# Performance work log

Measured on AMD Instinct MI355X. Metric: run time of the kernel, lower is better.

Reference implementation:

```python
import jax, jax.numpy as jnp
import numpy as np

B, SEQ, V = 8, 2048, 4096
D, H, DH, NL, FF = 1024, 16, 64, 8, 4096
MAXLEN = 4096
ATTN_EPS = 1e-6


def setup_inputs() -> dict:
    key = jax.random.key(0)
    ks = iter(jax.random.split(key, 40))
    w = lambda *s: jax.random.normal(next(ks), s, jnp.float32) * 0.02
    z = lambda *s: jnp.zeros(s, jnp.float32)
    o = lambda *s: jnp.ones(s, jnp.float32)
    return {
        'inputs': jax.random.uniform(next(ks), (B, SEQ, V), jnp.float32),
        'We': w(V, D), 'be': z(D),          # embedding Linear (stored [in,out])
        'pos': w(MAXLEN, D),                # positional embedding table
        'Wq': w(NL, D, D), 'bq': z(NL, D),
        'Wk': w(NL, D, D), 'bk': z(NL, D),
        'Wv': w(NL, D, D), 'bv': z(NL, D),
        'Wo': w(NL, D, D), 'bo': z(NL, D),
        'ln1g': o(NL, D), 'ln1b': z(NL, D),
        'W1': w(NL, D, FF), 'b1': z(NL, FF),
        'W2': w(NL, FF, D), 'b2': z(NL, D),
        'ln2g': o(NL, D), 'ln2b': z(NL, D),
        'gN': o(D), 'bN': z(D),
        'Wout': w(D, V), 'bout': z(V),
    }


def _rotate_half(u):
    u1, u2 = jnp.split(u, 2, axis=-1)
    return jnp.concatenate([-u2, u1], axis=-1)


def _ln(u, g, b, eps=1e-5):
    m = u.mean(-1, keepdims=True)
    var = ((u - m) ** 2).mean(-1, keepdims=True)
    return (u - m) * jax.lax.rsqrt(var + eps) * g + b


def _forward(inputs, We, be, pos, Wq, bq, Wk, bk, Wv, bv, Wo, bo,
             ln1g, ln1b, W1, b1, W2, b2, ln2g, ln2b, gN, bN, Wout, bout):
    N, S, Vv = inputs.shape
    T = S + 1
    # CLS one-hot prepended (last vocab slot reserved for CLS)
    cls = jnp.zeros((N, 1, Vv), inputs.dtype).at[:, :, Vv - 1].set(1.0)
    x = jnp.concatenate([cls, inputs], axis=1)       # [N,T,V]
    x = x @ We + be + pos[:T][None]                  # [N,T,D]

    # rotary tables for head_dim DH
    inv_freq = 1.0 / (10000.0 ** (jnp.arange(0, DH, 2, dtype=jnp.float32) / DH))
    freqs = jnp.arange(T, dtype=jnp.float32)[:, None] * inv_freq[None, :]
    emb = jnp.concatenate([freqs, freqs], axis=-1)   # [T,DH]
    cos = jnp.cos(emb)[None, :, None, :]
    sin = jnp.sin(emb)[None, :, None, :]

    def layer(x, p):
        wq, bq_, wk, bk_, wv, bv_, wo, bo_, g1, b1_, w1, bf1, w2, bf2, g2, b2_ = p
        q = (x @ wq + bq_).reshape(N, T, H, DH)
        k = (x @ wk + bk_).reshape(N, T, H, DH)
        v = (x @ wv + bv_).reshape(N, T, H, DH)
        q = q * cos + _rotate_half(q) * sin
        k = k * cos + _rotate_half(k) * sin
        # linear (kernelized) attention: phi(x) = elu(x) + 1, non-causal
        Qf = jax.nn.elu(q) + 1.0
        Kf = jax.nn.elu(k) + 1.0
        KV = jnp.einsum('nshd,nshm->nhdm', Kf, v)            # [N,H,DH,DH]
        Z = 1.0 / (jnp.einsum('nlhd,nhd->nlh', Qf, Kf.sum(1)) + ATTN_EPS)
        attn = jnp.einsum('nlhd,nhdm,nlh->nlhm', Qf, KV, Z).reshape(N, T, D)
        x = _ln(x + attn @ wo + bo_, g1, b1_)
        ff = jax.nn.gelu(x @ w1 + bf1, approximate=False) @ w2 + bf2
        x = _ln(x + ff, g2, b2_)
        return x, None

    params = (Wq, bq, Wk, bk, Wv, bv, Wo, bo, ln1g, ln1b, W1, b1, W2, b2, ln2g, ln2b)
    x, _ = jax.lax.scan(layer, x, params)
    x = _ln(x, gN, bN)
    return x[:, 0] @ Wout + bout                     # [N,V]


def reference(inputs, We, be, pos, Wq, bq, Wk, bk, Wv, bv, Wo, bo,
              ln1g, ln1b, W1, b1, W2, b2, ln2g, ln2b, gN, bN, Wout, bout):
    return _forward(inputs, We, be, pos, Wq, bq, Wk, bk, Wv, bv, Wo, bo,
                    ln1g, ln1b, W1, b1, W2, b2, ln2g, ln2b, gN, bN, Wout, bout)
```

## Files before the change

kernel.cpp:

```cpp
#include <hip/hip_runtime.h>
#include <math.h>

#define NB 8
#define SEQ 2048
#define V 4096
#define D 1024
#define H 16
#define DH 64
#define NL 8
#define FF 4096
#define TVAL 2049
#define MVAL (NB*TVAL)
#define MPAD 16512
#define TS 2112

typedef unsigned short u16;
typedef __attribute__((ext_vector_type(8))) __bf16 bfrag;
typedef __attribute__((ext_vector_type(4))) float f32x4;
typedef __attribute__((ext_vector_type(8))) unsigned short us8;
typedef __attribute__((ext_vector_type(4))) float fvec4;

__device__ __forceinline__ float b2f(u16 u) {
  union { unsigned int i; float f; } x; x.i = ((unsigned int)u) << 16; return x.f;
}
__device__ __forceinline__ u16 f2b(float f) {
  union { float f; unsigned int i; } x; x.f = f;
  unsigned int r = x.i + 0x7FFFu + ((x.i >> 16) & 1u);
  return (u16)(r >> 16);
}
__device__ __forceinline__ float phi_fn(float x) { return x > 0.f ? x + 1.f : __expf(x); }

__device__ __forceinline__ void async16(const u16* g, u16* l) {
  auto gp = (const __attribute__((address_space(1))) unsigned int*)(unsigned long long)g;
  auto lp = (__attribute__((address_space(3))) unsigned int*)(unsigned int)(unsigned long long)l;
  __builtin_amdgcn_global_load_lds(gp, lp, 16, 0, 0);
}

__device__ __forceinline__ f32x4 mfma16(bfrag a, bfrag b, f32x4 c) {
  return __builtin_amdgcn_mfma_f32_16x16x32_bf16(a, b, c, 0, 0, 0);
}


__global__ __launch_bounds__(256) void conv_kernel(const float* __restrict__ src,
                                                   u16* __restrict__ dst, long n) {
  long i = ((long)blockIdx.x * 256 + threadIdx.x) * 4;
  if (i < n) {
    fvec4 v = *(const fvec4*)(src + i);
    u16 o[4];
    #pragma unroll
    for (int j = 0; j < 4; ++j) o[j] = f2b(v[j]);
    *(uint2*)(dst + i) = *(const uint2*)o;
  }
}

__global__ __launch_bounds__(256) void transposeW(const float* __restrict__ src,
                                                  u16* __restrict__ dst, int K, int N) {
  const int z = blockIdx.z;
  src += (size_t)z * K * N;
  dst += (size_t)z * K * N;
  const int k0 = blockIdx.x * 64, n0 = blockIdx.y * 64;
  __shared__ __align__(16) u16 t[64][65];
  const int c = threadIdx.x & 63, r4 = threadIdx.x >> 6;
  #pragma unroll 4
  for (int i = 0; i < 16; ++i) {
    int k = i * 4 + r4;
    t[c][k] = f2b(src[(size_t)(k0 + k) * N + n0 + c]);
  }
  __syncthreads();
  #pragma unroll 4
  for (int i = 0; i < 16; ++i) {
    int nr = i * 4 + r4;
    dst[(size_t)(n0 + nr) * K + k0 + c] = t[nr][c];
  }
}

__global__ __launch_bounds__(256) void rope_table(float* __restrict__ ct, float* __restrict__ snt) {
  int idx = blockIdx.x * 256 + threadIdx.x;
  if (idx < TVAL * 32) {
    int s = idx >> 5, p = idx & 31;
    float ang = (float)s * powf(10000.f, -(float)p / 32.f);
    ct[idx] = cosf(ang);
    snt[idx] = sinf(ang);
  }
}

__global__ __launch_bounds__(256) void cls_kernel(const float* __restrict__ We,
                                                  const float* __restrict__ be,
                                                  const float* __restrict__ pos,
                                                  u16* __restrict__ xb, float* __restrict__ xf) {
  int n = blockIdx.x;
  for (int c = threadIdx.x; c < D; c += 256) {
    float v = We[(size_t)(V - 1) * D + c] + be[c] + pos[c];
    size_t idx = (size_t)(n * TVAL) * D + c;
    xb[idx] = f2b(v);
    xf[idx] = v;
  }
}

template<int EPI>
__global__ __launch_bounds__(256) void gemm_bt(
    const u16* __restrict__ A, const u16* __restrict__ Bt,
    const float* __restrict__ bias, const float* __restrict__ resf,
    const float* __restrict__ pos, u16* __restrict__ Cb, float* __restrict__ Cf,
    int N, int K) {
  __shared__ __align__(16) u16 sA[4096];
  __shared__ __align__(16) u16 sB[4096];
  const int tid = threadIdx.x, wave = tid >> 6, lane = tid & 63;
  const int fr = lane & 15, fc8 = (lane >> 4) << 3;
  const int rA = blockIdx.y * 128, rB = blockIdx.x * 128;
  const u16* gA0 = A + (size_t)(rA + wave * 16 + fr) * K + fc8;
  const u16* gA1 = A + (size_t)(rA + 64 + wave * 16 + fr) * K + fc8;
  const u16* gB0 = Bt + (size_t)(rB + wave * 16 + fr) * K + fc8;
  const u16* gB1 = Bt + (size_t)(rB + 64 + wave * 16 + fr) * K + fc8;
  u16* lA0 = sA + wave * 512;
  u16* lA1 = sA + (4 + wave) * 512;
  u16* lB0 = sB + wave * 512;
  u16* lB1 = sB + (4 + wave) * 512;
  const int wm = wave & 1, wn = wave >> 1;
  f32x4 acc[4][4];
  #pragma unroll
  for (int mt = 0; mt < 4; ++mt)
    #pragma unroll
    for (int nt = 0; nt < 4; ++nt)
      #pragma unroll
      for (int r = 0; r < 4; ++r) acc[mt][nt][r] = 0.f;

  for (int kk = 0; kk < K; kk += 32) {
    __syncthreads();
    async16(gA0 + kk, lA0);
    async16(gA1 + kk, lA1);
    async16(gB0 + kk, lB0);
    async16(gB1 + kk, lB1);
    __syncthreads();
    bfrag af[4], bfr[4];
    #pragma unroll
    for (int t = 0; t < 4; ++t) af[t] = *(const bfrag*)(sA + (wm * 4 + t) * 512 + lane * 8);
    #pragma unroll
    for (int t = 0; t < 4; ++t) bfr[t] = *(const bfrag*)(sB + (wn * 4 + t) * 512 + lane * 8);
    #pragma unroll
    for (int mt = 0; mt < 4; ++mt)
      #pragma unroll
      for (int nt = 0; nt < 4; ++nt)
        acc[mt][nt] = mfma16(af[mt], bfr[nt], acc[mt][nt]);
  }

  const int r0 = rA + wm * 64;
  const int c0 = rB + wn * 64;
  #pragma unroll
  for (int mt = 0; mt < 4; ++mt) {
    #pragma unroll
    for (int nt = 0; nt < 4; ++nt) {
      int col = c0 + nt * 16 + fr;
      float bi = bias[col];
      f32x4 v = acc[mt][nt];
      #pragma unroll
      for (int r = 0; r < 4; ++r) {
        int row = r0 + mt * 16 + ((lane >> 4) << 2) + r;
        float val = v[r] + bi;
        if (EPI == 0) {
          int bidx = row >> 11;
          int s = row & 2047;
          size_t orow = (size_t)bidx * TVAL + s + 1;
          float tt = val + pos[(size_t)(s + 1) * D + col];
          Cb[orow * D + col] = f2b(tt);
          Cf[orow * D + col] = tt;
        } else if (EPI == 1) {
          Cb[(size_t)row * N + col] = f2b(val);
        } else if (EPI == 2) {
          Cf[(size_t)row * N + col] = val + resf[(size_t)row * N + col];
        } else {
          float gl = 0.5f * val * (1.f + erff(val * 0.70710678118f));
          Cb[(size_t)row * N + col] = f2b(gl);
        }
      }
    }
  }
}

__global__ __launch_bounds__(256) void rope_kernel(
    u16* qb, const u16* __restrict__ kb, const u16* __restrict__ vb,
    u16* __restrict__ Kt, u16* __restrict__ Vt,
    const float* __restrict__ ct, const float* __restrict__ snt) {
  const int stile = blockIdx.x, h = blockIdx.y, n = blockIdx.z;
  const int tid = threadIdx.x;
  const int sl = tid >> 2;
  const int g8 = (tid & 3) << 3;
  const int s = stile * 64 + sl;
  const bool valid = s < TVAL;
  const size_t row = (size_t)n * TVAL + s;
  float ql[8], qh[8], kl[8], kh[8];
  us8 vlo = {0,0,0,0,0,0,0,0}, vhi = {0,0,0,0,0,0,0,0};
  if (valid) {
    const u16* qp = qb + row * D + (size_t)h * DH;
    const u16* kp = kb + row * D + (size_t)h * DH;
    const u16* vp = vb + row * D + (size_t)h * DH;
    us8 a = *(const us8*)(qp + g8);
    us8 b = *(const us8*)(qp + 32 + g8);
    us8 c = *(const us8*)(kp + g8);
    us8 d = *(const us8*)(kp + 32 + g8);
    vlo = *(const us8*)(vp + g8);
    vhi = *(const us8*)(vp + 32 + g8);
    #pragma unroll
    for (int j = 0; j < 8; ++j) {
      ql[j] = b2f(a[j]); qh[j] = b2f(b[j]);
      kl[j] = b2f(c[j]); kh[j] = b2f(d[j]);
    }
  } else {
    #pragma unroll
    for (int j = 0; j < 8; ++j) { ql[j] = qh[j] = kl[j] = kh[j] = 0.f; }
  }
  const int se = valid ? s : 0;
  us8 qolo, qohi;
  u16 kolo[8], kohi[8];
  #pragma unroll
  for (int j = 0; j < 8; ++j) {
    float c = ct[se * 32 + g8 + j];
    float sn = snt[se * 32 + g8 + j];
    float x1 = ql[j] * c - qh[j] * sn;
    float x2 = qh[j] * c + ql[j] * sn;
    qolo[j] = f2b(phi_fn(x1));
    qohi[j] = f2b(phi_fn(x2));
    float y1 = kl[j] * c - kh[j] * sn;
    float y2 = kh[j] * c + kl[j] * sn;
    kolo[j] = f2b(phi_fn(y1));
    kohi[j] = f2b(phi_fn(y2));
  }
  if (valid) {
    u16* qp = qb + row * D + (size_t)h * DH;
    *(us8*)(qp + g8) = qolo;
    *(us8*)(qp + 32 + g8) = qohi;
  }
  __shared__ __align__(16) u16 tile[64][72];
  #pragma unroll
  for (int j = 0; j < 8; ++j) {
    tile[g8 + j][sl] = valid ? kolo[j] : (u16)0;
    tile[32 + g8 + j][sl] = valid ? kohi[j] : (u16)0;
  }
  __syncthreads();
  {
    const int dr = tid >> 2, ck = (tid & 3) << 4;
    const size_t ob = ((size_t)(n * H + h) * DH + dr) * TS + (size_t)stile * 64 + ck;
    us8 t0 = *(const us8*)&tile[dr][ck];
    us8 t1 = *(const us8*)&tile[dr][ck + 8];
    *(us8*)(Kt + ob) = t0;
    *(us8*)(Kt + ob + 8) = t1;
  }
  __syncthreads();
  #pragma unroll
  for (int j = 0; j < 8; ++j) {
    tile[g8 + j][sl] = valid ? vlo[j] : (u16)0;
    tile[32 + g8 + j][sl] = valid ? vhi[j] : (u16)0;
  }
  __syncthreads();
  {
    const int dr = tid >> 2, ck = (tid & 3) << 4;
    const size_t ob = ((size_t)(n * H + h) * DH + dr) * TS + (size_t)stile * 64 + ck;
    us8 t0 = *(const us8*)&tile[dr][ck];
    us8 t1 = *(const us8*)&tile[dr][ck + 8];
    *(us8*)(Vt + ob) = t0;
    *(us8*)(Vt + ob + 8) = t1;
  }
}

__global__ __launch_bounds__(256) void kv_kernel(
    const u16* __restrict__ Kt, const u16* __restrict__ Vt,
    u16* __restrict__ KVt, float* __restrict__ Ksum) {
  const int nh = blockIdx.x;
  const int tid = threadIdx.x, wave = tid >> 6, lane = tid & 63;
  const size_t base = (size_t)nh * DH * TS;
  const int fr = lane & 15, fc = (lane >> 4) << 3;
  f32x4 acc[4][4];
  #pragma unroll
  for (int a = 0; a < 4; ++a)
    #pragma unroll
    for (int b = 0; b < 4; ++b)
      #pragma unroll
      for (int r = 0; r < 4; ++r) acc[a][b][r] = 0.f;
  for (int c = wave; c < TS / 32; c += 4) {
    const int s0 = c * 32 + fc;
    bfrag av[4], bk[4];
    #pragma unroll
    for (int t = 0; t < 4; ++t) {
      av[t] = *(const bfrag*)(Vt + base + (size_t)(t * 16 + fr) * TS + s0);
      bk[t] = *(const bfrag*)(Kt + base + (size_t)(t * 16 + fr) * TS + s0);
    }
    #pragma unroll
    for (int mt = 0; mt < 4; ++mt)
      #pragma unroll
      for (int dt = 0; dt < 4; ++dt)
        acc[mt][dt] = mfma16(av[mt], bk[dt], acc[mt][dt]);
  }
  __shared__ float red[4096];
  for (int i = tid; i < 4096; i += 256) red[i] = 0.f;
  __syncthreads();
  #pragma unroll
  for (int mt = 0; mt < 4; ++mt)
    #pragma unroll
    for (int dt = 0; dt < 4; ++dt)
      #pragma unroll
      for (int r = 0; r < 4; ++r) {
        int m = mt * 16 + ((lane >> 4) << 2) + r;
        int dd = dt * 16 + fr;
        atomicAdd(&red[m * 64 + dd], acc[mt][dt][r]);
      }
  __syncthreads();
  for (int i = tid; i < 4096; i += 256) KVt[(size_t)nh * 4096 + i] = f2b(red[i]);
  float ks = 0.f;
  const int dd = tid & 63, part = tid >> 6;
  for (int s = part * (TS / 4); s < (part + 1) * (TS / 4); s += 8) {
    us8 t = *(const us8*)(Kt + base + (size_t)dd * TS + s);
    #pragma unroll
    for (int j = 0; j < 8; ++j) ks += b2f(t[j]);
  }
  __shared__ float ksr[64];
  if (tid < 64) ksr[tid] = 0.f;
  __syncthreads();
  atomicAdd(&ksr[dd], ks);
  __syncthreads();
  if (tid < 64) Ksum[nh * 64 + tid] = ksr[tid];
}

__global__ __launch_bounds__(256) void z_kernel(const u16* __restrict__ qb,
                                                const float* __restrict__ Ksum,
                                                float* __restrict__ Z) {
  const int tid = threadIdx.x;
  const int row = blockIdx.x * 16 + (tid >> 4);
  const int h = tid & 15;
  if (row >= MVAL) return;
  const int n = row / TVAL;
  const u16* qp = qb + (size_t)row * D + h * DH;
  const float* kp = Ksum + (size_t)(n * 16 + h) * 64;
  float acc = 0.f;
  #pragma unroll
  for (int j = 0; j < 64; j += 8) {
    us8 t = *(const us8*)(qp + j);
    #pragma unroll
    for (int j2 = 0; j2 < 8; ++j2) acc += b2f(t[j2]) * kp[j + j2];
  }
  Z[(size_t)row * 16 + h] = 1.f / (acc + 1e-6f);
}

__global__ __launch_bounds__(256) void attn_kernel(
    const u16* __restrict__ qb, const u16* __restrict__ KVt,
    const float* __restrict__ Z, u16* __restrict__ attnb) {
  const int mt5 = blockIdx.x, nh = blockIdx.y, n = nh >> 4, h = nh & 15;
  const int tid = threadIdx.x, wave = tid >> 6, lane = tid & 63;
  const int fr = lane & 15, fc = (lane >> 4) << 3;
  f32x4 acc[2][4];
  #pragma unroll
  for (int a = 0; a < 2; ++a)
    #pragma unroll
    for (int b = 0; b < 4; ++b)
      #pragma unroll
      for (int r = 0; r < 4; ++r) acc[a][b][r] = 0.f;
  #pragma unroll
  for (int kc = 0; kc < 2; ++kc) {
    bfrag aq[2], bkv[4];
    #pragma unroll
    for (int m2 = 0; m2 < 2; ++m2) {
      int sr = mt5 * 128 + wave * 32 + m2 * 16 + fr;
      if (sr > 2048) sr = 2048;
      aq[m2] = *(const bfrag*)(qb + ((size_t)n * TVAL + sr) * D + h * DH + kc * 32 + fc);
    }
    #pragma unroll
    for (int nt = 0; nt < 4; ++nt)
      bkv[nt] = *(const bfrag*)(KVt + (size_t)nh * 4096 + (nt * 16 + fr) * 64 + kc * 32 + fc);
    #pragma unroll
    for (int m2 = 0; m2 < 2; ++m2)
      #pragma unroll
      for (int nt = 0; nt < 4; ++nt)
        acc[m2][nt] = mfma16(aq[m2], bkv[nt], acc[m2][nt]);
  }
  #pragma unroll
  for (int m2 = 0; m2 < 2; ++m2)
    #pragma unroll
    for (int nt = 0; nt < 4; ++nt)
      #pragma unroll
      for (int r = 0; r < 4; ++r) {
        int s = mt5 * 128 + wave * 32 + m2 * 16 + ((lane >> 4) << 2) + r;
        if (s < TVAL) {
          size_t row = (size_t)n * TVAL + s;
          float z = Z[row * 16 + h];
          attnb[row * D + h * DH + nt * 16 + fr] = f2b(acc[m2][nt][r] * z);
        }
      }
}

template<bool WF>
__global__ __launch_bounds__(256) void ln_kernel(const float* in, const float* __restrict__ g,
                                                 const float* __restrict__ b,
                                                 u16* __restrict__ ob, float* of) {
  const int tid = threadIdx.x, wave = tid >> 6, lane = tid & 63;
  const size_t row = (size_t)blockIdx.x * 4 + wave;
  const float* rp = in + row * D + lane * 16;
  float v[16];
  #pragma unroll
  for (int i = 0; i < 16; i += 4) {
    fvec4 t = *(const fvec4*)(rp + i);
    v[i] = t[0]; v[i + 1] = t[1]; v[i + 2] = t[2]; v[i + 3] = t[3];
  }
  float s = 0.f, s2 = 0.f;
  #pragma unroll
  for (int i = 0; i < 16; ++i) { s += v[i]; s2 += v[i] * v[i]; }
  #pragma unroll
  for (int m = 1; m < 64; m <<= 1) { s += __shfl_xor(s, m); s2 += __shfl_xor(s2, m); }
  float mean = s * (1.f / 1024.f);
  float var = s2 * (1.f / 1024.f) - mean * mean;
  float rstd = rsqrtf(var + 1e-5f);
  const int c0 = lane * 16;
  us8 o0, o1;
  #pragma unroll
  for (int i = 0; i < 16; ++i) {
    float o = (v[i] - mean) * rstd * g[c0 + i] + b[c0 + i];
    if (i < 8) o0[i] = f2b(o); else o1[i - 8] = f2b(o);
    if (WF) of[row * D + c0 + i] = o;
  }
  *(us8*)(ob + row * D + c0) = o0;
  *(us8*)(ob + row * D + c0 + 8) = o1;
}

__global__ __launch_bounds__(256) void lnf_kernel(const float* __restrict__ xf,
                                                  const float* __restrict__ gN,
                                                  const float* __restrict__ bN,
                                                  float* __restrict__ lnf) {
  const int n = blockIdx.x, tid = threadIdx.x;
  const float* rp = xf + (size_t)n * TVAL * D;
  float v[4];
  #pragma unroll
  for (int i = 0; i < 4; ++i) v[i] = rp[tid * 4 + i];
  float s = v[0] + v[1] + v[2] + v[3];
  float s2 = v[0]*v[0] + v[1]*v[1] + v[2]*v[2] + v[3]*v[3];
  #pragma unroll
  for (int m = 1; m < 64; m <<= 1) { s += __shfl_xor(s, m); s2 += __shfl_xor(s2, m); }
  __shared__ float rs[4], rs2[4];
  const int wave = tid >> 6, lane = tid & 63;
  if (lane == 0) { rs[wave] = s; rs2[wave] = s2; }
  __syncthreads();
  s = rs[0] + rs[1] + rs[2] + rs[3];
  s2 = rs2[0] + rs2[1] + rs2[2] + rs2[3];
  float mean = s * (1.f / 1024.f);
  float var = s2 * (1.f / 1024.f) - mean * mean;
  float rstd = rsqrtf(var + 1e-5f);
  #pragma unroll
  for (int i = 0; i < 4; ++i) {
    int c = tid * 4 + i;
    lnf[n * D + c] = (v[i] - mean) * rstd * gN[c] + bN[c];
  }
}

__global__ __launch_bounds__(256) void out_kernel(const float* __restrict__ lnf,
                                                  const float* __restrict__ Wout,
                                                  const float* __restrict__ bout,
                                                  float* __restrict__ out) {
  __shared__ float xs[8 * 1024];
  for (int i = threadIdx.x; i < 8192; i += 256) xs[i] = lnf[i];
  __syncthreads();
  const int j = blockIdx.x * 256 + threadIdx.x;
  float acc[8];
  float bj = bout[j];
  #pragma unroll
  for (int n = 0; n < 8; ++n) acc[n] = bj;
  for (int k = 0; k < 1024; ++k) {
    float w = Wout[(size_t)k * 4096 + j];
    #pragma unroll
    for (int n = 0; n < 8; ++n) acc[n] += xs[n * 1024 + k] * w;
  }
  #pragma unroll
  for (int n = 0; n < 8; ++n) out[(size_t)n * 4096 + j] = acc[n];
}

extern "C" void kernel_launch(void* const* d_in, const int* in_sizes, int n_in,
                              void* d_out, int out_size, void* d_ws, size_t ws_size,
                              hipStream_t stream) {
  const float* inputs = (const float*)d_in[0];
  const float* We   = (const float*)d_in[1];
  const float* be   = (const float*)d_in[2];
  const float* pos  = (const float*)d_in[3];
  const float* Wq   = (const float*)d_in[4];
  const float* bq   = (const float*)d_in[5];
  const float* Wk   = (const float*)d_in[6];
  const float* bk   = (const float*)d_in[7];
  const float* Wv   = (const float*)d_in[8];
  const float* bv   = (const float*)d_in[9];
  const float* Wo   = (const float*)d_in[10];
  const float* bo   = (const float*)d_in[11];
  const float* ln1g = (const float*)d_in[12];
  const float* ln1b = (const float*)d_in[13];
  const float* W1   = (const float*)d_in[14];
  const float* b1   = (const float*)d_in[15];
  const float* W2   = (const float*)d_in[16];
  const float* b2   = (const float*)d_in[17];
  const float* ln2g = (const float*)d_in[18];
  const float* ln2b = (const float*)d_in[19];
  const float* gN   = (const float*)d_in[20];
  const float* bN   = (const float*)d_in[21];
  const float* Wout = (const float*)d_in[22];
  const float* bout = (const float*)d_in[23];
  float* out = (float*)d_out;

  char* p = (char*)d_ws;
  auto alloc = [&](size_t b) { char* r = p; p += (b + 255) & ~(size_t)255; return r; };
  u16*   xb   = (u16*)alloc((size_t)MPAD * D * 2);
  float* xf   = (float*)alloc((size_t)MPAD * D * 4);
  float* hf   = (float*)alloc((size_t)MPAD * D * 4);
  u16*   qb   = (u16*)alloc((size_t)MPAD * D * 2);
  u16*   kb   = (u16*)alloc((size_t)MPAD * D * 2);
  u16*   vb   = (u16*)alloc((size_t)MPAD * D * 2);
  u16*   Kt   = (u16*)alloc((size_t)128 * DH * TS * 2);
  u16*   Vt   = (u16*)alloc((size_t)128 * DH * TS * 2);
  u16*   ffb  = (u16*)alloc((size_t)MPAD * FF * 2);
  u16*   inb  = ffb;
  u16*   WeT  = (u16*)alloc((size_t)V * D * 2);
  u16*   WqT  = (u16*)alloc((size_t)D * D * 2);
  u16*   WkT  = (u16*)alloc((size_t)D * D * 2);
  u16*   WvT  = (u16*)alloc((size_t)D * D * 2);
  u16*   WoT  = (u16*)alloc((size_t)D * D * 2);
  u16*   W1T  = (u16*)alloc((size_t)D * FF * 2);
  u16*   W2T  = (u16*)alloc((size_t)FF * D * 2);
  u16*   KVt  = (u16*)alloc((size_t)128 * 64 * 64 * 2);
  float* Ksum = (float*)alloc((size_t)128 * 64 * 4);
  float* Zb   = (float*)alloc((size_t)MPAD * 16 * 4);
  float* ct   = (float*)alloc((size_t)TVAL * 32 * 4);
  float* snt  = (float*)alloc((size_t)TVAL * 32 * 4);
  float* lnf  = (float*)alloc((size_t)8 * D * 4);

  hipMemsetAsync(Kt, 0, (size_t)128 * DH * TS * 2, stream);
  hipMemsetAsync(Vt, 0, (size_t)128 * DH * TS * 2, stream);
  rope_table<<<(TVAL * 32 + 255) / 256, 256, 0, stream>>>(ct, snt);
  conv_kernel<<<65536, 256, 0, stream>>>(inputs, inb, (long)NB * SEQ * V);
  transposeW<<<dim3(V / 64, D / 64, 1), 256, 0, stream>>>(We, WeT, V, D);
  cls_kernel<<<8, 256, 0, stream>>>(We, be, pos, xb, xf);
  gemm_bt<0><<<dim3(D / 128, 16384 / 128), 256, 0, stream>>>(
      inb, WeT, be, nullptr, pos, xb, xf, D, V);

  for (int l = 0; l < NL; ++l) {
    transposeW<<<dim3(16, 16, 1), 256, 0, stream>>>(Wq + (size_t)l * D * D, WqT, D, D);
    transposeW<<<dim3(16, 16, 1), 256, 0, stream>>>(Wk + (size_t)l * D * D, WkT, D, D);
    transposeW<<<dim3(16, 16, 1), 256, 0, stream>>>(Wv + (size_t)l * D * D, WvT, D, D);
    transposeW<<<dim3(16, 16, 1), 256, 0, stream>>>(Wo + (size_t)l * D * D, WoT, D, D);
    transposeW<<<dim3(16, 64, 1), 256, 0, stream>>>(W1 + (size_t)l * D * FF, W1T, D, FF);
    transposeW<<<dim3(64, 16, 1), 256, 0, stream>>>(W2 + (size_t)l * FF * D, W2T, FF, D);

    gemm_bt<1><<<dim3(8, 129), 256, 0, stream>>>(xb, WqT, bq + l * D, nullptr, nullptr, qb, nullptr, D, D);
    gemm_bt<1><<<dim3(8, 129), 256, 0, stream>>>(xb, WkT, bk + l * D, nullptr, nullptr, kb, nullptr, D, D);
    gemm_bt<1><<<dim3(8, 129), 256, 0, stream>>>(xb, WvT, bv + l * D, nullptr, nullptr, vb, nullptr, D, D);
    rope_kernel<<<dim3(33, 16, 8), 256, 0, stream>>>(qb, kb, vb, Kt, Vt, ct, snt);
    kv_kernel<<<128, 256, 0, stream>>>(Kt, Vt, KVt, Ksum);
    z_kernel<<<(MVAL + 15) / 16, 256, 0, stream>>>(qb, Ksum, Zb);
    attn_kernel<<<dim3(17, 128), 256, 0, stream>>>(qb, KVt, Zb, vb);
    gemm_bt<2><<<dim3(8, 129), 256, 0, stream>>>(vb, WoT, bo + l * D, xf, nullptr, nullptr, hf, D, D);
    ln_kernel<true><<<MPAD / 4, 256, 0, stream>>>(hf, ln1g + l * D, ln1b + l * D, qb, xf);
    gemm_bt<3><<<dim3(32, 129), 256, 0, stream>>>(qb, W1T, b1 + l * FF, nullptr, nullptr, ffb, nullptr, FF, D);
    gemm_bt<2><<<dim3(8, 129), 256, 0, stream>>>(ffb, W2T, b2 + l * D, xf, nullptr, nullptr, hf, D, FF);
    ln_kernel<true><<<MPAD / 4, 256, 0, stream>>>(hf, ln2g + l * D, ln2b + l * D, xb, xf);
  }

  lnf_kernel<<<8, 256, 0, stream>>>(xf, gN, bN, lnf);
  out_kernel<<<16, 256, 0, stream>>>(lnf, Wout, bout, out);
}
```

Before: 11.59 ms.

## Fuse QKV projections into one GEMM and double the GEMM K-step

Concatenates the transposed Wq/Wk/Wv weights and their biases so one GEMM writes a packed [M,3072] QKV buffer. Downstream rope, z, attention, output projection and layernorm kernels read and write that buffer through a row stride, and the attention output reuses the V slot. The GEMM also loads a 64-wide K slab per sync instead of 32, doubling shared memory to halve barrier count. This cuts kernel launches and per-iteration sync overhead, but the larger LDS footprint may reduce occupancy and the strided A rows add some access overhead.

Result: faster. 10.87 ms (-6.2%).

```diff
diff --git a/kernel.cpp b/kernel.cpp
--- a/kernel.cpp
+++ b/kernel.cpp
@@ -13,6 +13,7 @@
 #define MVAL (NB*TVAL)
 #define MPAD 16512
 #define TS 2112
+#define QS 3072
 
 typedef unsigned short u16;
 typedef __attribute__((ext_vector_type(8))) __bf16 bfrag;
@@ -84,6 +85,19 @@
   }
 }
 
+__global__ __launch_bounds__(256) void pack_bias(const float* __restrict__ bq,
+                                                 const float* __restrict__ bk,
+                                                 const float* __restrict__ bv,
+                                                 float* __restrict__ bqkv) {
+  int i = blockIdx.x * 256 + threadIdx.x;
+  if (i >= NL * QS) return;
+  int l = i / QS, j = i - l * QS;
+  float v = (j < 1024) ? bq[l * 1024 + j]
+          : (j < 2048) ? bk[l * 1024 + j - 1024]
+                       : bv[l * 1024 + j - 2048];
+  bqkv[i] = v;
+}
+
 __global__ __launch_bounds__(256) void cls_kernel(const float* __restrict__ We,
                                                   const float* __restrict__ be,
                                                   const float* __restrict__ pos,
@@ -102,14 +116,14 @@
     const u16* __restrict__ A, const u16* __restrict__ Bt,
     const float* __restrict__ bias, const float* __restrict__ resf,
     const float* __restrict__ pos, u16* __restrict__ Cb, float* __restrict__ Cf,
-    int N, int K) {
-  __shared__ __align__(16) u16 sA[4096];
-  __shared__ __align__(16) u16 sB[4096];
+    int N, int K, int lda) {
+  __shared__ __align__(16) u16 sA[8192];
+  __shared__ __align__(16) u16 sB[8192];
   const int tid = threadIdx.x, wave = tid >> 6, lane = tid & 63;
   const int fr = lane & 15, fc8 = (lane >> 4) << 3;
   const int rA = blockIdx.y * 128, rB = blockIdx.x * 128;
-  const u16* gA0 = A + (size_t)(rA + wave * 16 + fr) * K + fc8;
-  const u16* gA1 = A + (size_t)(rA + 64 + wave * 16 + fr) * K + fc8;
+  const u16* gA0 = A + (size_t)(rA + wave * 16 + fr) * lda + fc8;
+  const u16* gA1 = A + (size_t)(rA + 64 + wave * 16 + fr) * lda + fc8;
   const u16* gB0 = Bt + (size_t)(rB + wave * 16 + fr) * K + fc8;
   const u16* gB1 = Bt + (size_t)(rB + 64 + wave * 16 + fr) * K + fc8;
   u16* lA0 = sA + wave * 512;
@@ -125,23 +139,31 @@
       #pragma unroll
       for (int r = 0; r < 4; ++r) acc[mt][nt][r] = 0.f;
 
-  for (int kk = 0; kk < K; kk += 32) {
+  for (int kk = 0; kk < K; kk += 64) {
     __syncthreads();
-    async16(gA0 + kk, lA0);
-    async16(gA1 + kk, lA1);
-    async16(gB0 + kk, lB0);
-    async16(gB1 + kk, lB1);
+    #pragma unroll
+    for (int h = 0; h < 2; ++h) {
+      async16(gA0 + kk + 32 * h, lA0 + 4096 * h);
+      async16(gA1 + kk + 32 * h, lA1 + 4096 * h);
+      async16(gB0 + kk + 32 * h, lB0 + 4096 * h);
+      async16(gB1 + kk + 32 * h, lB1 + 4096 * h);
+    }
     __syncthreads();
-    bfrag af[4], bfr[4];
-    #pragma unroll
-    for (int t = 0; t < 4; ++t) af[t] = *(const bfrag*)(sA + (wm * 4 + t) * 512 + lane * 8);
-    #pragma unroll
-    for (int t = 0; t < 4; ++t) bfr[t] = *(const bfrag*)(sB + (wn * 4 + t) * 512 + lane * 8);
-    #pragma unroll
-    for (int mt = 0; mt < 4; ++mt)
-      #pragma unroll
-      for (int nt = 0; nt < 4; ++nt)
-        acc[mt][nt] = mfma16(af[mt], bfr[nt], acc[mt][nt]);
+    #pragma unroll
+    for (int h = 0; h < 2; ++h) {
+      bfrag af[4], bfr[4];
+      #pragma unroll
+      for (int t = 0; t < 4; ++t)
+        af[t] = *(const bfrag*)(sA + h * 4096 + (wm * 4 + t) * 512 + lane * 8);
+      #pragma unroll
+      for (int t = 0; t < 4; ++t)
+        bfr[t] = *(const bfrag*)(sB + h * 4096 + (wn * 4 + t) * 512 + lane * 8);
+      #pragma unroll
+      for (int mt = 0; mt < 4; ++mt)
+        #pragma unroll
+        for (int nt = 0; nt < 4; ++nt)
+          acc[mt][nt] = mfma16(af[mt], bfr[nt], acc[mt][nt]);
+    }
   }
 
   const int r0 = rA + wm * 64;
@@ -178,8 +200,7 @@
 }
 
 __global__ __launch_bounds__(256) void rope_kernel(
-    u16* qb, const u16* __restrict__ kb, const u16* __restrict__ vb,
-    u16* __restrict__ Kt, u16* __restrict__ Vt,
+    u16* qkv, u16* __restrict__ Kt, u16* __restrict__ Vt,
     const float* __restrict__ ct, const float* __restrict__ snt) {
   const int stile = blockIdx.x, h = blockIdx.y, n = blockIdx.z;
   const int tid = threadIdx.x;
@@ -191,9 +212,9 @@
   float ql[8], qh[8], kl[8], kh[8];
   us8 vlo = {0,0,0,0,0,0,0,0}, vhi = {0,0,0,0,0,0,0,0};
   if (valid) {
-    const u16* qp = qb + row * D + (size_t)h * DH;
-    const u16* kp = kb + row * D + (size_t)h * DH;
-    const u16* vp = vb + row * D + (size_t)h * DH;
+    const u16* qp = qkv + row * QS + (size_t)h * DH;
+    const u16* kp = qkv + row * QS + 1024 + (size_t)h * DH;
+    const u16* vp = qkv + row * QS + 2048 + (size_t)h * DH;
     us8 a = *(const us8*)(qp + g8);
     us8 b = *(const us8*)(qp + 32 + g8);
     us8 c = *(const us8*)(kp + g8);
@@ -226,7 +247,7 @@
     kohi[j] = f2b(phi_fn(y2));
   }
   if (valid) {
-    u16* qp = qb + row * D + (size_t)h * DH;
+    u16* qp = qkv + row * QS + (size_t)h * DH;
     *(us8*)(qp + g8) = qolo;
     *(us8*)(qp + 32 + g8) = qohi;
   }
@@ -320,7 +341,7 @@
   if (tid < 64) Ksum[nh * 64 + tid] = ksr[tid];
 }
 
-__global__ __launch_bounds__(256) void z_kernel(const u16* __restrict__ qb,
+__global__ __launch_bounds__(256) void z_kernel(const u16* __restrict__ qkv,
                                                 const float* __restrict__ Ksum,
                                                 float* __restrict__ Z) {
   const int tid = threadIdx.x;
@@ -328,7 +349,7 @@
   const int h = tid & 15;
   if (row >= MVAL) return;
   const int n = row / TVAL;
-  const u16* qp = qb + (size_t)row * D + h * DH;
+  const u16* qp = qkv + (size_t)row * QS + h * DH;
   const float* kp = Ksum + (size_t)(n * 16 + h) * 64;
   float acc = 0.f;
   #pragma unroll
@@ -341,8 +362,8 @@
 }
 
 __global__ __launch_bounds__(256) void attn_kernel(
-    const u16* __restrict__ qb, const u16* __restrict__ KVt,
-    const float* __restrict__ Z, u16* __restrict__ attnb) {
+    u16* qkv, const u16* __restrict__ KVt,
+    const float* __restrict__ Z) {
   const int mt5 = blockIdx.x, nh = blockIdx.y, n = nh >> 4, h = nh & 15;
   const int tid = threadIdx.x, wave = tid >> 6, lane = tid & 63;
   const int fr = lane & 15, fc = (lane >> 4) << 3;
@@ -360,7 +381,7 @@
     for (int m2 = 0; m2 < 2; ++m2) {
       int sr = mt5 * 128 + wave * 32 + m2 * 16 + fr;
       if (sr > 2048) sr = 2048;
-      aq[m2] = *(const bfrag*)(qb + ((size_t)n * TVAL + sr) * D + h * DH + kc * 32 + fc);
+      aq[m2] = *(const bfrag*)(qkv + ((size_t)n * TVAL + sr) * QS + h * DH + kc * 32 + fc);
     }
     #pragma unroll
     for (int nt = 0; nt < 4; ++nt)
@@ -381,7 +402,7 @@
         if (s < TVAL) {
           size_t row = (size_t)n * TVAL + s;
           float z = Z[row * 16 + h];
-          attnb[row * D + h * DH + nt * 16 + fr] = f2b(acc[m2][nt][r] * z);
+          qkv[row * QS + 2048 + h * DH + nt * 16 + fr] = f2b(acc[m2][nt][r] * z);
         }
       }
 }
@@ -389,7 +410,7 @@
 template<bool WF>
 __global__ __launch_bounds__(256) void ln_kernel(const float* in, const float* __restrict__ g,
                                                  const float* __restrict__ b,
-                                                 u16* __restrict__ ob, float* of) {
+                                                 u16* __restrict__ ob, int ostride, float* of) {
   const int tid = threadIdx.x, wave = tid >> 6, lane = tid & 63;
   const size_t row = (size_t)blockIdx.x * 4 + wave;
   const float* rp = in + row * D + lane * 16;
@@ -415,8 +436,8 @@
     if (i < 8) o0[i] = f2b(o); else o1[i - 8] = f2b(o);
     if (WF) of[row * D + c0 + i] = o;
   }
-  *(us8*)(ob + row * D + c0) = o0;
-  *(us8*)(ob + row * D + c0 + 8) = o1;
+  *(us8*)(ob + row * (size_t)ostride + c0) = o0;
+  *(us8*)(ob + row * (size_t)ostride + c0 + 8) = o1;
 }
 
 __global__ __launch_bounds__(256) void lnf_kernel(const float* __restrict__ xf,
@@ -503,17 +524,13 @@
   u16*   xb   = (u16*)alloc((size_t)MPAD * D * 2);
   float* xf   = (float*)alloc((size_t)MPAD * D * 4);
   float* hf   = (float*)alloc((size_t)MPAD * D * 4);
-  u16*   qb   = (u16*)alloc((size_t)MPAD * D * 2);
-  u16*   kb   = (u16*)alloc((size_t)MPAD * D * 2);
-  u16*   vb   = (u16*)alloc((size_t)MPAD * D * 2);
+  u16*   qkvb = (u16*)alloc((size_t)MPAD * QS * 2);
   u16*   Kt   = (u16*)alloc((size_t)128 * DH * TS * 2);
   u16*   Vt   = (u16*)alloc((size_t)128 * DH * TS * 2);
   u16*   ffb  = (u16*)alloc((size_t)MPAD * FF * 2);
   u16*   inb  = ffb;
   u16*   WeT  = (u16*)alloc((size_t)V * D * 2);
-  u16*   WqT  = (u16*)alloc((size_t)D * D * 2);
-  u16*   WkT  = (u16*)alloc((size_t)D * D * 2);
-  u16*   WvT  = (u16*)alloc((size_t)D * D * 2);
+  u16*   WqkvT= (u16*)alloc((size_t)QS * D * 2);
   u16*   WoT  = (u16*)alloc((size_t)D * D * 2);
   u16*   W1T  = (u16*)alloc((size_t)D * FF * 2);
   u16*   W2T  = (u16*)alloc((size_t)FF * D * 2);
@@ -523,36 +540,40 @@
   float* ct   = (float*)alloc((size_t)TVAL * 32 * 4);
   float* snt  = (float*)alloc((size_t)TVAL * 32 * 4);
   float* lnf  = (float*)alloc((size_t)8 * D * 4);
+  float* bqkv = (float*)alloc((size_t)NL * QS * 4);
 
   hipMemsetAsync(Kt, 0, (size_t)128 * DH * TS * 2, stream);
   hipMemsetAsync(Vt, 0, (size_t)128 * DH * TS * 2, stream);
   rope_table<<<(TVAL * 32 + 255) / 256, 256, 0, stream>>>(ct, snt);
+  pack_bias<<<(NL * QS + 255) / 256, 256, 0, stream>>>(bq, bk, bv, bqkv);
   conv_kernel<<<65536, 256, 0, stream>>>(inputs, inb, (long)NB * SEQ * V);
   transposeW<<<dim3(V / 64, D / 64, 1), 256, 0, stream>>>(We, WeT, V, D);
   cls_kernel<<<8, 256, 0, stream>>>(We, be, pos, xb, xf);
   gemm_bt<0><<<dim3(D / 128, 16384 / 128), 256, 0, stream>>>(
-      inb, WeT, be, nullptr, pos, xb, xf, D, V);
+      inb, WeT, be, nullptr, pos, xb, xf, D, V, V);
 
   for (int l = 0; l < NL; ++l) {
-    transposeW<<<dim3(16, 16, 1), 256, 0, stream>>>(Wq + (size_t)l * D * D, WqT, D, D);
-    transposeW<<<dim3(16, 16, 1), 256, 0, stream>>>(Wk + (size_t)l * D * D, WkT, D, D);
-    transposeW<<<dim3(16, 16, 1), 256, 0, stream>>>(Wv + (size_t)l * D * D, WvT, D, D);
+    transposeW<<<dim3(16, 16, 1), 256, 0, stream>>>(Wq + (size_t)l * D * D, WqkvT, D, D);
+    transposeW<<<dim3(16, 16, 1), 256, 0, stream>>>(Wk + (size_t)l * D * D, WqkvT + (size_t)1024 * D, D, D);
+    transposeW<<<dim3(16, 16, 1), 256, 0, stream>>>(Wv + (size_t)l * D * D, WqkvT + (size_t)2048 * D, D, D);
     transposeW<<<dim3(16, 16, 1), 256, 0, stream>>>(Wo + (size_t)l * D * D, WoT, D, D);
     transposeW<<<dim3(16, 64, 1), 256, 0, stream>>>(W1 + (size_t)l * D * FF, W1T, D, FF);
     transposeW<<<dim3(64, 16, 1), 256, 0, stream>>>(W2 + (size_t)l * FF * D, W2T, FF, D);
 
-    gemm_bt<1><<<dim3(8, 129), 256, 0, stream>>>(xb, WqT, bq + l * D, nullptr, nullptr, qb, nullptr, D, D);
-    gemm_bt<1><<<dim3(8, 129), 256, 0, stream>>>(xb, WkT, bk + l * D, nullptr, nullptr, kb, nullptr, D, D);
-    gemm_bt<1><<<dim3(8, 129), 256, 0, stream>>>(xb, WvT, bv + l * D, nullptr, nullptr, vb, nullptr, D, D);
-    rope_kernel<<<dim3(33, 16, 8), 256, 0, stream>>>(qb, kb, vb, Kt, Vt, ct, snt);
+    gemm_bt<1><<<dim3(24, 129), 256, 0, stream>>>(xb, WqkvT, bqkv + l * QS, nullptr, nullptr,
+                                                  qkvb, nullptr, QS, D, D);
+    rope_kernel<<<dim3(33, 16, 8), 256, 0, stream>>>(qkvb, Kt, Vt, ct, snt);
     kv_kernel<<<128, 256, 0, stream>>>(Kt, Vt, KVt, Ksum);
-    z_kernel<<<(MVAL + 15) / 16, 256, 0, stream>>>(qb, Ksum, Zb);
-    attn_kernel<<<dim3(17, 128), 256, 0, stream>>>(qb, KVt, Zb, vb);
-    gemm_bt<2><<<dim3(8, 129), 256, 0, stream>>>(vb, WoT, bo + l * D, xf, nullptr, nullptr, hf, D, D);
-    ln_kernel<true><<<MPAD / 4, 256, 0, stream>>>(hf, ln1g + l * D, ln1b + l * D, qb, xf);
-    gemm_bt<3><<<dim3(32, 129), 256, 0, stream>>>(qb, W1T, b1 + l * FF, nullptr, nullptr, ffb, nullptr, FF, D);
-    gemm_bt<2><<<dim3(8, 129), 256, 0, stream>>>(ffb, W2T, b2 + l * D, xf, nullptr, nullptr, hf, D, FF);
-    ln_kernel<true><<<MPAD / 4, 256, 0, stream>>>(hf, ln2g + l * D, ln2b + l * D, xb, xf);
+    z_kernel<<<(MVAL + 15) / 16, 256, 0, stream>>>(qkvb, Ksum, Zb);
+    attn_kernel<<<dim3(17, 128), 256, 0, stream>>>(qkvb, KVt, Zb);
+    gemm_bt<2><<<dim3(8, 129), 256, 0, stream>>>(qkvb + 2048, WoT, bo + l * D, xf, nullptr,
+                                                 nullptr, hf, D, D, QS);
+    ln_kernel<true><<<MPAD / 4, 256, 0, stream>>>(hf, ln1g + l * D, ln1b + l * D, qkvb, QS, xf);
+    gemm_bt<3><<<dim3(32, 129), 256, 0, stream>>>(qkvb, W1T, b1 + l * FF, nullptr, nullptr,
+                                                  ffb, nullptr, FF, D, QS);
+    gemm_bt<2><<<dim3(8, 129), 256, 0, stream>>>(ffb, W2T, b2 + l * D, xf, nullptr,
+                                                 nullptr, hf, D, FF, FF);
+    ln_kernel<true><<<MPAD / 4, 256, 0, stream>>>(hf, ln2g + l * D, ln2b + l * D, xb, D, xf);
   }
 
   lnf_kernel<<<8, 256, 0, stream>>>(xf, gN, bN, lnf);
```
